# Performance work log

Measured on AMD Instinct MI355X. Metric: run time of the kernel, lower is better.

## Reference

```python
import jax, jax.numpy as jnp
import numpy as np

N = 768      # sentence length n
E = 256      # embedding_dim (== 2*H so layer inputs stack)
H = 128      # lstm_hidden_dim
NL = 2       # lstm_num_layers
F = 128      # fc_hidden_dim


def _run_dir(x, Wih, Whh, b):
    """One LSTM direction over x:(T, in). PyTorch gate order i,f,g,o."""
    pre = x @ Wih.T + b  # (T, 4H), precomputed input contribution
    Hd = Whh.shape[1]
    def step(carry, p):
        h, c = carry
        g = p + Whh @ h
        i, f, gg, o = jnp.split(g, 4)
        i = jax.nn.sigmoid(i)
        f = jax.nn.sigmoid(f)
        gg = jnp.tanh(gg)
        o = jax.nn.sigmoid(o)
        c = f * c + i * gg
        h = o * jnp.tanh(c)
        return (h, c), h
    h0 = jnp.zeros((Hd,), x.dtype)
    _, hs = jax.lax.scan(step, (h0, h0), pre)
    return hs  # (T, H)


def _bilstm(x, Wih, Whh, bih, bhh):
    # Wih: (NL, 2, 4H, in), eval mode (no inter-layer dropout)
    for l in range(Wih.shape[0]):
        hf = _run_dir(x, Wih[l, 0], Whh[l, 0], bih[l, 0] + bhh[l, 0])
        hb = jnp.flip(_run_dir(jnp.flip(x, 0), Wih[l, 1], Whh[l, 1], bih[l, 1] + bhh[l, 1]), 0)
        x = jnp.concatenate([hf, hb], axis=-1)  # (T, 2H)
    return x


def setup_inputs() -> dict:
    key = jax.random.key(0)
    ks = jax.random.split(key, 12)
    s = 0.08
    return {
        "sentence_embedded": jax.random.normal(ks[0], (N, E), jnp.float32),
        "deps": jax.random.randint(ks[1], (N,), 0, N + 1),
        "root_vec": jax.random.uniform(ks[2], (1, E), jnp.float32),
        "Wih": jax.random.normal(ks[3], (NL, 2, 4 * H, E), jnp.float32) * s,
        "Whh": jax.random.normal(ks[4], (NL, 2, 4 * H, H), jnp.float32) * s,
        "bih": jax.random.normal(ks[5], (NL, 2, 4 * H), jnp.float32) * s,
        "bhh": jax.random.normal(ks[6], (NL, 2, 4 * H), jnp.float32) * s,
        "W1": jax.random.normal(ks[7], (F, 4 * H), jnp.float32) * s,
        "b1": jax.random.normal(ks[8], (F,), jnp.float32) * s,
        "w2": jax.random.normal(ks[9], (F,), jnp.float32) * s,
        "b2": jax.random.normal(ks[10], (1,), jnp.float32) * s,
    }


def reference(sentence_embedded, deps, root_vec, Wih, Whh, bih, bhh, W1, b1, w2, b2):
    n = sentence_embedded.shape[0]
    x = jnp.concatenate([sentence_embedded, root_vec], axis=0)  # (n+1, E)
    L = _bilstm(x, Wih, Whh, bih, bhh)                          # (n+1, 2H)
    d = L.shape[1]
    # mlp(concat(L[i], L[j])) computed for all pairs by splitting fc1:
    # fc1(concat(a,b)) = a @ W1a.T + b @ W1b.T + b1
    W1a, W1b = W1[:, :d], W1[:, d:]
    A = L @ W1a.T          # (n+1, F) head-side projection
    B = L[:n] @ W1b.T      # (n, F)   dependent-side projection
    Hact = jnp.tanh(A[:, None, :] + B[None, :, :] + b1)  # (n+1, n, F)
    scores = Hact @ w2 + b2[0]                           # (n+1, n)
    # diagonal (i == j, i < n) set to -inf as in the torch loop
    mask = jnp.arange(n + 1)[:, None] == jnp.arange(n)[None, :]
    return jnp.where(mask, -jnp.inf, scores)
```

## Files before the change

kernel.cpp:

```cpp
#include <hip/hip_runtime.h>
#include <hip/hip_fp8.h>

#define T_SEQ 769
#define N_SENT 768
#define E_IN 256
#define HID 128
#define G4 512
#define F_DIM 128

typedef float f32x4 __attribute__((ext_vector_type(4)));
typedef int i32x8 __attribute__((ext_vector_type(8)));

#if __has_builtin(__builtin_amdgcn_rcpf)
#define RCPF(x) __builtin_amdgcn_rcpf(x)
#else
#define RCPF(x) (1.0f / (x))
#endif

#if __has_builtin(__builtin_amdgcn_exp2f)
#define EXP2F(x) __builtin_amdgcn_exp2f(x)
#else
#define EXP2F(x) __builtin_exp2f(x)
#endif

#define LDS_BARRIER() asm volatile("s_waitcnt lgkmcnt(0)\n\ts_barrier" ::: "memory")

#define L2E 1.4426950408889634f

__device__ __forceinline__ float tanh_fast(float x) {
    return fmaf(2.0f, RCPF(1.0f + EXP2F(-2.0f * L2E * x)), -1.0f);
}

__device__ __forceinline__ unsigned char f32_to_e4m3(float x) {
#if __has_builtin(__builtin_amdgcn_cvt_pk_fp8_f32)
    return (unsigned char)(__builtin_amdgcn_cvt_pk_fp8_f32(x, x, 0, false) & 0xFF);
#else
    __hip_fp8_e4m3 q(x);
    return (unsigned char)q.__x;
#endif
}

__device__ __forceinline__ int pack4_e4m3(float w0, float w1, float w2, float w3) {
#if __has_builtin(__builtin_amdgcn_cvt_pk_fp8_f32)
    int r = __builtin_amdgcn_cvt_pk_fp8_f32(w0, w1, 0, false);
    return __builtin_amdgcn_cvt_pk_fp8_f32(w2, w3, r, true);
#else
    unsigned x = 0;
    __hip_fp8_e4m3 q0(w0), q1(w1), q2(w2), q3(w3);
    x |= (unsigned)q0.__x;
    x |= (unsigned)q1.__x << 8;
    x |= (unsigned)q2.__x << 16;
    x |= (unsigned)q3.__x << 24;
    return (int)x;
#endif
}

__device__ __forceinline__ float quad_bcast(float x, const int sel) {
#if __has_builtin(__builtin_amdgcn_mov_dpp)
    int ctrl = sel * 0x55;
    int r;
    switch (ctrl) {
        case 0x00: r = __builtin_amdgcn_mov_dpp(__float_as_int(x), 0x00, 0xF, 0xF, true); break;
        case 0x55: r = __builtin_amdgcn_mov_dpp(__float_as_int(x), 0x55, 0xF, 0xF, true); break;
        case 0xAA: r = __builtin_amdgcn_mov_dpp(__float_as_int(x), 0xAA, 0xF, 0xF, true); break;
        default:   r = __builtin_amdgcn_mov_dpp(__float_as_int(x), 0xFF, 0xF, 0xF, true); break;
    }
    return __int_as_float(r);
#else
    int lane = __lane_id();
    return __shfl(x, (lane & ~3) + sel, 64);
#endif
}

__global__ __launch_bounds__(256) void pre_gemm_l0(
    const float* __restrict__ sent, const float* __restrict__ root,
    const float* __restrict__ Wih, const float* __restrict__ bih,
    const float* __restrict__ bhh, float* __restrict__ pre)
{
    const int d = blockIdx.z;
    const float* B = Wih + (size_t)d * G4 * E_IN;
    const float* b0 = bih + (size_t)d * G4;
    const float* b1 = bhh + (size_t)d * G4;
    float* C = pre + (size_t)d * T_SEQ * G4;

    __shared__ __align__(16) float As[16][68];
    __shared__ __align__(16) float Bs[16][68];
    int tid = threadIdx.x;
    int tx = tid & 15, ty = tid >> 4;
    int m0 = blockIdx.x * 64, n0 = blockIdx.y * 64;
    float acc[4][4] = {};
    int lrow = tid >> 2;
    int lk = (tid & 3) << 2;

    for (int k0 = 0; k0 < E_IN; k0 += 16) {
        int m = m0 + lrow;
        float4 av = make_float4(0.f, 0.f, 0.f, 0.f);
        if (m < T_SEQ) {
            int ar = d ? (N_SENT - m) : m;
            av = (ar < N_SENT)
                     ? *(const float4*)(sent + (size_t)ar * E_IN + k0 + lk)
                     : *(const float4*)(root + k0 + lk);
        }
        As[lk + 0][lrow] = av.x; As[lk + 1][lrow] = av.y;
        As[lk + 2][lrow] = av.z; As[lk + 3][lrow] = av.w;
        float4 bv = *(const float4*)(B + (size_t)(n0 + lrow) * E_IN + k0 + lk);
        Bs[lk + 0][lrow] = bv.x; Bs[lk + 1][lrow] = bv.y;
        Bs[lk + 2][lrow] = bv.z; Bs[lk + 3][lrow] = bv.w;
        __syncthreads();
        #pragma unroll
        for (int k = 0; k < 16; ++k) {
            float4 a4 = *(const float4*)&As[k][ty * 4];
            float4 b4 = *(const float4*)&Bs[k][tx * 4];
            float aa[4] = {a4.x, a4.y, a4.z, a4.w};
            float bb[4] = {b4.x, b4.y, b4.z, b4.w};
            #pragma unroll
            for (int i = 0; i < 4; ++i)
                #pragma unroll
                for (int j = 0; j < 4; ++j)
                    acc[i][j] = fmaf(aa[i], bb[j], acc[i][j]);
        }
        __syncthreads();
    }
    float bias[4];
    #pragma unroll
    for (int j = 0; j < 4; ++j) {
        int n = n0 + tx * 4 + j;
        bias[j] = b0[n] + b1[n];
    }
    #pragma unroll
    for (int i = 0; i < 4; ++i) {
        int m = m0 + ty * 4 + i;
        if (m < T_SEQ) {
            #pragma unroll
            for (int j = 0; j < 4; ++j)
                C[(size_t)m * G4 + n0 + tx * 4 + j] = acc[i][j] + bias[j];
        }
    }
}

__global__ __launch_bounds__(256) void pre_gemm_l1(
    const float* __restrict__ L0,
    const float* __restrict__ Wih, const float* __restrict__ bih,
    const float* __restrict__ bhh, float* __restrict__ pre)
{
    const int d = blockIdx.z;
    const float* B = Wih + (size_t)(2 + d) * G4 * E_IN;
    const float* b0 = bih + (size_t)(2 + d) * G4;
    const float* b1 = bhh + (size_t)(2 + d) * G4;
    float* C = pre + (size_t)d * T_SEQ * G4;

    __shared__ __align__(16) float As[16][68];
    __shared__ __align__(16) float Bs[16][68];
    int tid = threadIdx.x;
    int tx = tid & 15, ty = tid >> 4;
    int m0 = blockIdx.x * 64, n0 = blockIdx.y * 64;
    float acc[4][4] = {};
    int lrow = tid >> 2;
    int lk = (tid & 3) << 2;

    for (int k0 = 0; k0 < 256; k0 += 16) {
        int m = m0 + lrow;
        float4 av = make_float4(0.f, 0.f, 0.f, 0.f);
        if (m < T_SEQ) {
            int ar = d ? (N_SENT - m) : m;
            av = *(const float4*)(L0 + (size_t)ar * 256 + k0 + lk);
        }
        As[lk + 0][lrow] = av.x; As[lk + 1][lrow] = av.y;
        As[lk + 2][lrow] = av.z; As[lk + 3][lrow] = av.w;
        float4 bv = *(const float4*)(B + (size_t)(n0 + lrow) * 256 + k0 + lk);
        Bs[lk + 0][lrow] = bv.x; Bs[lk + 1][lrow] = bv.y;
        Bs[lk + 2][lrow] = bv.z; Bs[lk + 3][lrow] = bv.w;
        __syncthreads();
        #pragma unroll
        for (int k = 0; k < 16; ++k) {
            float4 a4 = *(const float4*)&As[k][ty * 4];
            float4 b4 = *(const float4*)&Bs[k][tx * 4];
            float aa[4] = {a4.x, a4.y, a4.z, a4.w};
            float bb[4] = {b4.x, b4.y, b4.z, b4.w};
            #pragma unroll
            for (int i = 0; i < 4; ++i)
                #pragma unroll
                for (int j = 0; j < 4; ++j)
                    acc[i][j] = fmaf(aa[i], bb[j], acc[i][j]);
        }
        __syncthreads();
    }
    float bias[4];
    #pragma unroll
    for (int j = 0; j < 4; ++j) {
        int n = n0 + tx * 4 + j;
        bias[j] = b0[n] + b1[n];
    }
    #pragma unroll
    for (int i = 0; i < 4; ++i) {
        int m = m0 + ty * 4 + i;
        if (m < T_SEQ) {
            #pragma unroll
            for (int j = 0; j < 4; ++j)
                C[(size_t)m * G4 + n0 + tx * 4 + j] = acc[i][j] + bias[j];
        }
    }
}

__global__ __launch_bounds__(256) void ab_gemm(
    const float* __restrict__ L1, const float* __restrict__ W1,
    const float* __restrict__ b1, float* __restrict__ Ap,
    float* __restrict__ Bm)
{
    const int z = blockIdx.z;
    const int M = z ? N_SENT : T_SEQ;
    const float* B = W1 + (z ? 256 : 0);
    float* C = z ? Bm : Ap;

    __shared__ __align__(16) float As[16][68];
    __shared__ __align__(16) float Bs[16][68];
    int tid = threadIdx.x;
    int tx = tid & 15, ty = tid >> 4;
    int m0 = blockIdx.x * 64, n0 = blockIdx.y * 64;
    float acc[4][4] = {};
    int lrow = tid >> 2;
    int lk = (tid & 3) << 2;

    for (int k0 = 0; k0 < 256; k0 += 16) {
        int m = m0 + lrow;
        float4 av = make_float4(0.f, 0.f, 0.f, 0.f);
        if (m < M) av = *(const float4*)(L1 + (size_t)m * 256 + k0 + lk);
        As[lk + 0][lrow] = av.x; As[lk + 1][lrow] = av.y;
        As[lk + 2][lrow] = av.z; As[lk + 3][lrow] = av.w;
        float4 bv = *(const float4*)(B + (size_t)(n0 + lrow) * 512 + k0 + lk);
        Bs[lk + 0][lrow] = bv.x; Bs[lk + 1][lrow] = bv.y;
        Bs[lk + 2][lrow] = bv.z; Bs[lk + 3][lrow] = bv.w;
        __syncthreads();
        #pragma unroll
        for (int k = 0; k < 16; ++k) {
            float4 a4 = *(const float4*)&As[k][ty * 4];
            float4 b4 = *(const float4*)&Bs[k][tx * 4];
            float aa[4] = {a4.x, a4.y, a4.z, a4.w};
            float bb[4] = {b4.x, b4.y, b4.z, b4.w};
            #pragma unroll
            for (int i = 0; i < 4; ++i)
                #pragma unroll
                for (int j = 0; j < 4; ++j)
                    acc[i][j] = fmaf(aa[i], bb[j], acc[i][j]);
        }
        __syncthreads();
    }
    float bias[4];
    #pragma unroll
    for (int j = 0; j < 4; ++j) {
        int n = n0 + tx * 4 + j;
        bias[j] = z ? 0.f : b1[n];
    }
    #pragma unroll
    for (int i = 0; i < 4; ++i) {
        int m = m0 + ty * 4 + i;
        if (m < M) {
            #pragma unroll
            for (int j = 0; j < 4; ++j)
                C[(size_t)m * F_DIM + n0 + tx * 4 + j] = acc[i][j] + bias[j];
        }
    }
}

__global__ __launch_bounds__(512)
__attribute__((amdgpu_waves_per_eu(2, 2)))
void lstm_layer(
    const float* __restrict__ pre,
    const float* __restrict__ Whh,
    float* __restrict__ L)
{
    const int d = blockIdx.x;
    const int t = threadIdx.x;
    const int wv = t >> 6;
    const int l = t & 63;
    const int g = l & 3;
    const int v = (l >> 2) & 3;
    const int q = l >> 4;
    const int u = wv * 16 + 4 * q + v;
    const int c15 = l & 15;

    __shared__ __align__(16) unsigned char hb[2][HID];

    i32x8 Bf[4];
    #pragma unroll
    for (int j = 0; j < 4; ++j) {
        int row = (c15 & 3) * HID + wv * 16 + 4 * j + (c15 >> 2);
        const float* wr = Whh + ((size_t)d * G4 + row) * HID + q * 32;
        i32x8 bv;
        #pragma unroll
        for (int w8 = 0; w8 < 8; ++w8) {
            bv[w8] = pack4_e4m3(wr[w8 * 4 + 0], wr[w8 * 4 + 1],
                                wr[w8 * 4 + 2], wr[w8 * 4 + 3]);
        }
        Bf[j] = bv;
    }

    if (t < HID) { hb[0][t] = 0; hb[1][t] = 0; }

    const float Ag = (g == 2) ? 2.0f : 1.0f;
    const float Bg = (g == 2) ? (-2.0f * L2E) : (-L2E);
    const float Cg = (g == 2) ? -1.0f : 0.0f;
    const bool qb0 = (q & 1) != 0;
    const bool qb1 = (q & 2) != 0;

    const float* pp = pre + (size_t)d * T_SEQ * G4;
    const int po = g * HID + u;
    float p0 = pp[po];            pp += G4;
    float p1v = pp[po];           pp += G4;
    float p2v = pp[po];           pp += G4;

    float* Lrow = L + (size_t)(d ? N_SENT : 0) * 256 + d * HID + u;
    const ptrdiff_t ldelta = d ? -(ptrdiff_t)256 : (ptrdiff_t)256;

    f32x4 a0 = {0.f, 0.f, 0.f, 0.f};
    f32x4 a1 = {0.f, 0.f, 0.f, 0.f};
    f32x4 a2 = {0.f, 0.f, 0.f, 0.f};
    f32x4 a3 = {0.f, 0.f, 0.f, 0.f};
    float c = 0.f;
    __syncthreads();

    #pragma unroll 4
    for (int s = 0; s < T_SEQ; ++s) {
        i32x8 Af = *(const i32x8*)&hb[s & 1][q * 32];

        float p3 = pp[po];
        pp += G4;

        a0[0] = p0; a1[0] = p0; a2[0] = p0; a3[0] = p0;
        a0 = __builtin_amdgcn_mfma_scale_f32_16x16x128_f8f6f4(
            Af, Bf[0], a0, 0, 0, 0, 0x7F7F7F7F, 0, 0x7F7F7F7F);
        a1 = __builtin_amdgcn_mfma_scale_f32_16x16x128_f8f6f4(
            Af, Bf[1], a1, 0, 0, 0, 0x7F7F7F7F, 0, 0x7F7F7F7F);
        a2 = __builtin_amdgcn_mfma_scale_f32_16x16x128_f8f6f4(
            Af, Bf[2], a2, 0, 0, 0, 0x7F7F7F7F, 0, 0x7F7F7F7F);
        a3 = __builtin_amdgcn_mfma_scale_f32_16x16x128_f8f6f4(
            Af, Bf[3], a3, 0, 0, 0, 0x7F7F7F7F, 0, 0x7F7F7F7F);

        float xa = qb0 ? a1[0] : a0[0];
        float xb = qb0 ? a3[0] : a2[0];
        float x = qb1 ? xb : xa;
        float act = fmaf(Ag, RCPF(1.0f + EXP2F(Bg * x)), Cg);

        float gi = quad_bcast(act, 0);
        float gf = quad_bcast(act, 1);
        float gg = quad_bcast(act, 2);
        float go = quad_bcast(act, 3);

        c = fmaf(gf, c, gi * gg);
        float R = RCPF(1.0f + EXP2F(-2.0f * L2E * c));
        float go2 = go + go;
        float h = fmaf(go2, R, -go);
        if (g == 0) {
            Lrow[0] = h;
            hb[(s + 1) & 1][u] = f32_to_e4m3(h);
        }
        Lrow += ldelta;
        p0 = p1v; p1v = p2v; p2v = p3;
        LDS_BARRIER();
    }
}

__global__ __launch_bounds__(256) void scores_k(
    const float* __restrict__ Ap,
    const float* __restrict__ Bm,
    const float* __restrict__ w2,
    const float* __restrict__ b2,
    float* __restrict__ out)
{
    __shared__ __align__(16) float Asl[32][132];
    __shared__ __align__(16) float Bsl[32][132];
    __shared__ __align__(16) float w2s[F_DIM];
    int tid = threadIdx.x;
    int i0 = blockIdx.x * 32, j0 = blockIdx.y * 32;

    for (int e = tid; e < 1024; e += 256) {
        int r = e >> 5;
        int qq = (e & 31) << 2;
        float4 av = (i0 + r < T_SEQ)
                        ? *(const float4*)(Ap + (size_t)(i0 + r) * F_DIM + qq)
                        : make_float4(0.f, 0.f, 0.f, 0.f);
        *(float4*)&Asl[r][qq] = av;
        float4 bv = *(const float4*)(Bm + (size_t)(j0 + r) * F_DIM + qq);
        *(float4*)&Bsl[r][qq] = bv;
    }
    if (tid < 32) {
        *(float4*)&w2s[tid * 4] = *(const float4*)(w2 + tid * 4);
    }
    __syncthreads();

    int tx = tid & 15, ty = tid >> 4;
    float s[2][2] = {};
    #pragma unroll 8
    for (int k4 = 0; k4 < F_DIM; k4 += 4) {
        float4 a0 = *(const float4*)&Asl[ty * 2][k4];
        float4 a1 = *(const float4*)&Asl[ty * 2 + 1][k4];
        float4 b0 = *(const float4*)&Bsl[tx * 2][k4];
        float4 b1v = *(const float4*)&Bsl[tx * 2 + 1][k4];
        float4 wv = *(const float4*)&w2s[k4];
        float aa[2][4] = {{a0.x, a0.y, a0.z, a0.w}, {a1.x, a1.y, a1.z, a1.w}};
        float bb[2][4] = {{b0.x, b0.y, b0.z, b0.w}, {b1v.x, b1v.y, b1v.z, b1v.w}};
        float ww[4] = {wv.x, wv.y, wv.z, wv.w};
        #pragma unroll
        for (int kk = 0; kk < 4; ++kk)
            #pragma unroll
            for (int ii = 0; ii < 2; ++ii)
                #pragma unroll
                for (int jj = 0; jj < 2; ++jj)
                    s[ii][jj] = fmaf(ww[kk],
                                     tanh_fast(aa[ii][kk] + bb[jj][kk]),
                                     s[ii][jj]);
    }

    float bb2 = b2[0];
    #pragma unroll
    for (int ii = 0; ii < 2; ++ii) {
        int i = i0 + ty * 2 + ii;
        if (i < T_SEQ) {
            #pragma unroll
            for (int jj = 0; jj < 2; ++jj) {
                int j = j0 + tx * 2 + jj;
                out[(size_t)i * N_SENT + j] =
                    (i == j) ? -1.0e30f : (s[ii][jj] + bb2);
            }
        }
    }
}

extern "C" void kernel_launch(void* const* d_in, const int* in_sizes, int n_in,
                              void* d_out, int out_size, void* d_ws, size_t ws_size,
                              hipStream_t stream) {
    const float* sent = (const float*)d_in[0];
    const float* root = (const float*)d_in[2];
    const float* Wih  = (const float*)d_in[3];
    const float* Whh  = (const float*)d_in[4];
    const float* bih  = (const float*)d_in[5];
    const float* bhh  = (const float*)d_in[6];
    const float* W1   = (const float*)d_in[7];
    const float* b1   = (const float*)d_in[8];
    const float* w2   = (const float*)d_in[9];
    const float* b2   = (const float*)d_in[10];
    float* out = (float*)d_out;
    float* ws = (float*)d_ws;

    float* pre = ws;
    float* L0  = pre + 2 * T_SEQ * G4;
    float* L1  = L0 + T_SEQ * 256;
    float* Ap  = L1 + T_SEQ * 256;
    float* Bm  = Ap + T_SEQ * F_DIM;

    dim3 b256(256);

    pre_gemm_l0<<<dim3(13, 8, 2), b256, 0, stream>>>(sent, root, Wih, bih, bhh, pre);
    lstm_layer<<<2, 512, 0, stream>>>(pre, Whh, L0);

    pre_gemm_l1<<<dim3(13, 8, 2), b256, 0, stream>>>(L0, Wih, bih, bhh, pre);
    lstm_layer<<<2, 512, 0, stream>>>(pre, Whh + (size_t)2 * G4 * HID, L1);

    ab_gemm<<<dim3(13, 2, 2), b256, 0, stream>>>(L1, W1, b1, Ap, Bm);

    scores_k<<<dim3(25, 24), b256, 0, stream>>>(Ap, Bm, w2, b2, out);
}
```

Baseline: 674.3 us.

## Halve LSTM block to 4 waves with two hidden units per lane

The recurrent LSTM kernel now runs with 256 threads (4 waves) instead of 512 (8 waves). Each wave holds twice the fp8 Whh fragments and issues eight MFMAs per step covering two hidden-unit groups. This reduces the number of waves that must meet at the per-timestep LDS barrier, which is meant to cut synchronisation latency on the serial recurrence. In exchange each wave has a longer dependent chain per step: more MFMAs, twice the activation work, and more registers in use.

```diff
diff --git a/kernel.cpp b/kernel.cpp
--- a/kernel.cpp
+++ b/kernel.cpp
@@ -262,8 +262,8 @@
     }
 }
 
-__global__ __launch_bounds__(512)
-__attribute__((amdgpu_waves_per_eu(2, 2)))
+__global__ __launch_bounds__(256)
+__attribute__((amdgpu_waves_per_eu(1, 1)))
 void lstm_layer(
     const float* __restrict__ pre,
     const float* __restrict__ Whh,
@@ -276,15 +276,16 @@
     const int g = l & 3;
     const int v = (l >> 2) & 3;
     const int q = l >> 4;
-    const int u = wv * 16 + 4 * q + v;
     const int c15 = l & 15;
+    const int u1 = wv * 32 + 4 * q + v;
+    const int u2 = u1 + 16;
 
     __shared__ __align__(16) unsigned char hb[2][HID];
 
-    i32x8 Bf[4];
-    #pragma unroll
-    for (int j = 0; j < 4; ++j) {
-        int row = (c15 & 3) * HID + wv * 16 + 4 * j + (c15 >> 2);
+    i32x8 Bf[8];
+    #pragma unroll
+    for (int j = 0; j < 8; ++j) {
+        int row = (c15 & 3) * HID + wv * 32 + (j >> 2) * 16 + (j & 3) * 4 + (c15 >> 2);
         const float* wr = Whh + ((size_t)d * G4 + row) * HID + q * 32;
         i32x8 bv;
         #pragma unroll
@@ -304,29 +305,34 @@
     const bool qb1 = (q & 2) != 0;
 
     const float* pp = pre + (size_t)d * T_SEQ * G4;
-    const int po = g * HID + u;
-    float p0 = pp[po];            pp += G4;
-    float p1v = pp[po];           pp += G4;
-    float p2v = pp[po];           pp += G4;
-
-    float* Lrow = L + (size_t)(d ? N_SENT : 0) * 256 + d * HID + u;
+    const int po = g * HID + u1;
+    float pA0 = pp[po], pB0 = pp[po + 16]; pp += G4;
+    float pA1 = pp[po], pB1 = pp[po + 16]; pp += G4;
+    float pA2 = pp[po], pB2 = pp[po + 16]; pp += G4;
+
+    float* Lrow = L + (size_t)(d ? N_SENT : 0) * 256 + d * HID;
     const ptrdiff_t ldelta = d ? -(ptrdiff_t)256 : (ptrdiff_t)256;
 
     f32x4 a0 = {0.f, 0.f, 0.f, 0.f};
     f32x4 a1 = {0.f, 0.f, 0.f, 0.f};
     f32x4 a2 = {0.f, 0.f, 0.f, 0.f};
     f32x4 a3 = {0.f, 0.f, 0.f, 0.f};
-    float c = 0.f;
+    f32x4 a4 = {0.f, 0.f, 0.f, 0.f};
+    f32x4 a5 = {0.f, 0.f, 0.f, 0.f};
+    f32x4 a6 = {0.f, 0.f, 0.f, 0.f};
+    f32x4 a7 = {0.f, 0.f, 0.f, 0.f};
+    float c1 = 0.f, c2 = 0.f;
     __syncthreads();
 
-    #pragma unroll 4
+    #pragma unroll 2
     for (int s = 0; s < T_SEQ; ++s) {
         i32x8 Af = *(const i32x8*)&hb[s & 1][q * 32];
 
-        float p3 = pp[po];
+        float pA3 = pp[po], pB3 = pp[po + 16];
         pp += G4;
 
-        a0[0] = p0; a1[0] = p0; a2[0] = p0; a3[0] = p0;
+        a0[0] = pA0; a1[0] = pA0; a2[0] = pA0; a3[0] = pA0;
+        a4[0] = pB0; a5[0] = pB0; a6[0] = pB0; a7[0] = pB0;
         a0 = __builtin_amdgcn_mfma_scale_f32_16x16x128_f8f6f4(
             Af, Bf[0], a0, 0, 0, 0, 0x7F7F7F7F, 0, 0x7F7F7F7F);
         a1 = __builtin_amdgcn_mfma_scale_f32_16x16x128_f8f6f4(
@@ -335,27 +341,51 @@
             Af, Bf[2], a2, 0, 0, 0, 0x7F7F7F7F, 0, 0x7F7F7F7F);
         a3 = __builtin_amdgcn_mfma_scale_f32_16x16x128_f8f6f4(
             Af, Bf[3], a3, 0, 0, 0, 0x7F7F7F7F, 0, 0x7F7F7F7F);
+        a4 = __builtin_amdgcn_mfma_scale_f32_16x16x128_f8f6f4(
+            Af, Bf[4], a4, 0, 0, 0, 0x7F7F7F7F, 0, 0x7F7F7F7F);
+        a5 = __builtin_amdgcn_mfma_scale_f32_16x16x128_f8f6f4(
+            Af, Bf[5], a5, 0, 0, 0, 0x7F7F7F7F, 0, 0x7F7F7F7F);
+        a6 = __builtin_amdgcn_mfma_scale_f32_16x16x128_f8f6f4(
+            Af, Bf[6], a6, 0, 0, 0, 0x7F7F7F7F, 0, 0x7F7F7F7F);
+        a7 = __builtin_amdgcn_mfma_scale_f32_16x16x128_f8f6f4(
+            Af, Bf[7], a7, 0, 0, 0, 0x7F7F7F7F, 0, 0x7F7F7F7F);
 
         float xa = qb0 ? a1[0] : a0[0];
         float xb = qb0 ? a3[0] : a2[0];
-        float x = qb1 ? xb : xa;
-        float act = fmaf(Ag, RCPF(1.0f + EXP2F(Bg * x)), Cg);
-
-        float gi = quad_bcast(act, 0);
-        float gf = quad_bcast(act, 1);
-        float gg = quad_bcast(act, 2);
-        float go = quad_bcast(act, 3);
-
-        c = fmaf(gf, c, gi * gg);
-        float R = RCPF(1.0f + EXP2F(-2.0f * L2E * c));
-        float go2 = go + go;
-        float h = fmaf(go2, R, -go);
-        if (g == 0) {
-            Lrow[0] = h;
-            hb[(s + 1) & 1][u] = f32_to_e4m3(h);
+        float x1 = qb1 ? xb : xa;
+        float xc = qb0 ? a5[0] : a4[0];
+        float xd = qb0 ? a7[0] : a6[0];
+        float x2 = qb1 ? xd : xc;
+
+        float act1 = fmaf(Ag, RCPF(1.0f + EXP2F(Bg * x1)), Cg);
+        float act2 = fmaf(Ag, RCPF(1.0f + EXP2F(Bg * x2)), Cg);
+
+        float gi1 = quad_bcast(act1, 0);
+        float gf1 = quad_bcast(act1, 1);
+        float gg1 = quad_bcast(act1, 2);
+        float go1 = quad_bcast(act1, 3);
+        float gi2 = quad_bcast(act2, 0);
+        float gf2 = quad_bcast(act2, 1);
+        float gg2 = quad_bcast(act2, 2);
+        float go2 = quad_bcast(act2, 3);
+
+        c1 = fmaf(gf1, c1, gi1 * gg1);
+        c2 = fmaf(gf2, c2, gi2 * gg2);
+        float R1 = RCPF(1.0f + EXP2F(-2.0f * L2E * c1));
+        float h1 = fmaf(go1 + go1, R1, -go1);
+        float R2 = RCPF(1.0f + EXP2F(-2.0f * L2E * c2));
+        float h2 = fmaf(go2 + go2, R2, -go2);
+
+        if (g < 2) {
+            int us = g ? u2 : u1;
+            float hs = g ? h2 : h1;
+            Lrow[us] = hs;
+            hb[(s + 1) & 1][us] = f32_to_e4m3(hs);
         }
         Lrow += ldelta;
-        p0 = p1v; p1v = p2v; p2v = p3;
+        pA0 = pA1; pB0 = pB1;
+        pA1 = pA2; pB1 = pB2;
+        pA2 = pA3; pB2 = pB3;
         LDS_BARRIER();
     }
 }
@@ -451,10 +481,10 @@
     dim3 b256(256);
 
     pre_gemm_l0<<<dim3(13, 8, 2), b256, 0, stream>>>(sent, root, Wih, bih, bhh, pre);
-    lstm_layer<<<2, 512, 0, stream>>>(pre, Whh, L0);
+    lstm_layer<<<2, 256, 0, stream>>>(pre, Whh, L0);
 
     pre_gemm_l1<<<dim3(13, 8, 2), b256, 0, stream>>>(L0, Wih, bih, bhh, pre);
-    lstm_layer<<<2, 512, 0, stream>>>(pre, Whh + (size_t)2 * G4 * HID, L1);
+    lstm_layer<<<2, 256, 0, stream>>>(pre, Whh + (size_t)2 * G4 * HID, L1);
 
     ab_gemm<<<dim3(13, 2, 2), b256, 0, stream>>>(L1, W1, b1, Ap, Bm);
 
```

After: 767.9 us. 13.9% more time.
